# Kernel tuning notes

Measured on AMD Instinct MI355X. Metric: run time of the kernel, lower is better.

Reference implementation:

```python
import jax, jax.numpy as jnp
import numpy as np

N_EMBD = 1024
HEAD_SIZE = 128


def setup_inputs() -> dict:
    key = jax.random.key(0)
    k_x, k_w, k_cov, k_b = jax.random.split(key, 4)
    x = jax.random.normal(k_x, (16384, 2, N_EMBD), dtype=jnp.float32)
    # values_proj: nn.Linear(n_embd, head_size, bias=False) -> weight [head_size, n_embd]
    W = jax.random.normal(k_w, (HEAD_SIZE, N_EMBD), dtype=jnp.float32) * (N_EMBD ** -0.5)
    cov = jax.random.normal(k_cov, (HEAD_SIZE, HEAD_SIZE), dtype=jnp.float32) * (HEAD_SIZE ** -0.5)
    bias = jax.random.normal(k_b, (HEAD_SIZE,), dtype=jnp.float32)
    return {"x": x, "W": W, "cov": cov, "bias": bias}


def reference(x, W, cov, bias):
    # x: [B, 2, E]; W: [H, E]; cov: [H, H]; bias: [H]
    values = jnp.einsum('be,he->bh', x[:, 0, :], W)  # [B, H]
    mask = jnp.einsum('be,he->bh', x[:, 1, :], W)    # [B, H]
    # diag_embed(mask) @ cov == mask[:, :, None] * cov  -> [B, H, H]
    coeffs = jax.nn.softmax(mask[:, :, None] * cov[None, :, :], axis=-1)
    # values.unsqueeze(1) @ coeffs + bias, then [:, 0, :]
    out = jnp.einsum('bh,bhk->bk', values, coeffs) + bias
    return out
```

## Files before the change

kernel.cpp:

```cpp
#include <hip/hip_runtime.h>
#include <hip/hip_bf16.h>

#define LOG2E 1.4426950408889634f

typedef __attribute__((ext_vector_type(8))) short frag_ab;
typedef __attribute__((ext_vector_type(4))) float frag_cd;

__device__ inline short f2bf(float f) {
    union { float f; unsigned u; } v; v.f = f;
    unsigned r = v.u + 0x7fffu + ((v.u >> 16) & 1u);
    return (short)(r >> 16);
}

__global__ __launch_bounds__(256) void prep_kernel(const float* __restrict__ W,
                                                   const float* __restrict__ cov,
                                                   short* __restrict__ wbf,
                                                   float* __restrict__ rmm) {
    if (blockIdx.x < 64) {
        int g = blockIdx.x * 256 + threadIdx.x;
        int h = g >> 7;
        int k0 = (g & 127) << 3;
        const float* src = W + h * 1024 + k0;
        float4 w0 = *(const float4*)src;
        float4 w1 = *(const float4*)(src + 4);
        frag_ab af;
        af[0] = f2bf(w0.x); af[1] = f2bf(w0.y); af[2] = f2bf(w0.z); af[3] = f2bf(w0.w);
        af[4] = f2bf(w1.x); af[5] = f2bf(w1.y); af[6] = f2bf(w1.z); af[7] = f2bf(w1.w);
        int c = k0 >> 6, s = (k0 >> 5) & 1, kg = (k0 >> 3) & 3;
        int nt = h >> 4, m = h & 15, lane = kg * 16 + m;
        int dst = (((c * 8 + nt) * 2 + s) * 64 + lane) * 8;
        *(frag_ab*)(wbf + dst) = af;
    } else {
        int h = blockIdx.x - 64;
        int lane = threadIdx.x;
        if (lane < 64) {
            float c1 = cov[h * 128 + lane];
            float c2 = cov[h * 128 + 64 + lane];
            float mx = fmaxf(c1, c2), mn = fminf(c1, c2);
            for (int o = 1; o < 64; o <<= 1) {
                mx = fmaxf(mx, __shfl_xor(mx, o, 64));
                mn = fminf(mn, __shfl_xor(mn, o, 64));
            }
            if (lane == 0) { rmm[h] = LOG2E * mx; rmm[128 + h] = LOG2E * mn; }
        }
    }
}

__global__ __launch_bounds__(256, 2) void proj_kernel(const float* __restrict__ x,
                                                      const short* __restrict__ wbf,
                                                      float* __restrict__ vm) {
    __shared__ __align__(16) short Bs[2][8192];
    const int tid = threadIdx.x;
    const int lane = tid & 63, wave = tid >> 6;
    const int m = lane & 15, kg = lane >> 4;
    const long rowbase = (long)blockIdx.x * 64 + wave * 16;
    const float* xrow = x + (rowbase + m) * 1024 + kg * 8;

    frag_cd acc[8];
#pragma unroll
    for (int nt = 0; nt < 8; ++nt) acc[nt] = (frag_cd){0.f, 0.f, 0.f, 0.f};

    {
        const char* wc = (const char*)wbf;
        float4 t0 = *(const float4*)(wc + tid * 16);
        float4 t1 = *(const float4*)(wc + 4096 + tid * 16);
        float4 t2 = *(const float4*)(wc + 8192 + tid * 16);
        float4 t3 = *(const float4*)(wc + 12288 + tid * 16);
        char* bd = (char*)&Bs[0][0] + tid * 16;
        *(float4*)(bd)         = t0;
        *(float4*)(bd + 4096)  = t1;
        *(float4*)(bd + 8192)  = t2;
        *(float4*)(bd + 12288) = t3;
    }
    float4 a0 = *(const float4*)(xrow);
    float4 a1 = *(const float4*)(xrow + 4);
    float4 a2 = *(const float4*)(xrow + 32);
    float4 a3 = *(const float4*)(xrow + 36);
    __syncthreads();

    int cb = 0;
    for (int c = 0; c < 16; ++c) {
        float4 n0, n1, n2, n3, B0, B1, B2, B3;
        if (c < 15) {
            const float* xn = xrow + (c + 1) * 64;
            n0 = *(const float4*)(xn);
            n1 = *(const float4*)(xn + 4);
            n2 = *(const float4*)(xn + 32);
            n3 = *(const float4*)(xn + 36);
            const char* wc = (const char*)wbf + (c + 1) * 16384;
            B0 = *(const float4*)(wc + tid * 16);
            B1 = *(const float4*)(wc + 4096 + tid * 16);
            B2 = *(const float4*)(wc + 8192 + tid * 16);
            B3 = *(const float4*)(wc + 12288 + tid * 16);
        }
        frag_ab af0, af1;
        af0[0] = f2bf(a0.x); af0[1] = f2bf(a0.y); af0[2] = f2bf(a0.z); af0[3] = f2bf(a0.w);
        af0[4] = f2bf(a1.x); af0[5] = f2bf(a1.y); af0[6] = f2bf(a1.z); af0[7] = f2bf(a1.w);
        af1[0] = f2bf(a2.x); af1[1] = f2bf(a2.y); af1[2] = f2bf(a2.z); af1[3] = f2bf(a2.w);
        af1[4] = f2bf(a3.x); af1[5] = f2bf(a3.y); af1[6] = f2bf(a3.z); af1[7] = f2bf(a3.w);

        const char* bs = (const char*)&Bs[cb][0];
#pragma unroll
        for (int nt = 0; nt < 8; ++nt) {
            frag_ab bf0 = *(const frag_ab*)(bs + (nt * 2 + 0) * 1024 + lane * 16);
            acc[nt] = __builtin_amdgcn_mfma_f32_16x16x32_bf16(af0, bf0, acc[nt], 0, 0, 0);
            frag_ab bf1 = *(const frag_ab*)(bs + (nt * 2 + 1) * 1024 + lane * 16);
            acc[nt] = __builtin_amdgcn_mfma_f32_16x16x32_bf16(af1, bf1, acc[nt], 0, 0, 0);
        }
        if (c < 15) {
            char* bd = (char*)&Bs[cb ^ 1][0] + tid * 16;
            *(float4*)(bd)         = B0;
            *(float4*)(bd + 4096)  = B1;
            *(float4*)(bd + 8192)  = B2;
            *(float4*)(bd + 12288) = B3;
            a0 = n0; a1 = n1; a2 = n2; a3 = n3;
        }
        __syncthreads();
        cb ^= 1;
    }

#pragma unroll
    for (int nt = 0; nt < 8; ++nt) {
#pragma unroll
        for (int r = 0; r < 4; ++r) {
            long row = rowbase + kg * 4 + r;
            vm[row * 128 + nt * 16 + m] = acc[nt][r];
        }
    }
}

__global__ __launch_bounds__(512, 4) void combine_kernel(const float* __restrict__ vm,
                                                         const float* __restrict__ cov,
                                                         const float* __restrict__ bias,
                                                         const float* __restrict__ rmm,
                                                         float* __restrict__ out, int B) {
    __shared__ float mask_s[128], m2_s[128], v_s[128];
    __shared__ float obuf[32][132];
    const int t = threadIdx.x;
    const int i = t >> 4;
    const int j = t & 15;

    float covreg[4][8];
#pragma unroll
    for (int hh = 0; hh < 4; ++hh) {
        const float* cr = cov + (long)(i * 4 + hh) * 128 + j * 8;
        float4 c0 = *(const float4*)cr;
        float4 c1 = *(const float4*)(cr + 4);
        covreg[hh][0] = LOG2E * c0.x; covreg[hh][1] = LOG2E * c0.y;
        covreg[hh][2] = LOG2E * c0.z; covreg[hh][3] = LOG2E * c0.w;
        covreg[hh][4] = LOG2E * c1.x; covreg[hh][5] = LOG2E * c1.y;
        covreg[hh][6] = LOG2E * c1.z; covreg[hh][7] = LOG2E * c1.w;
    }
    float rmax_own = 0.f, rmin_own = 0.f, bias_own = 0.f;
    if (t < 128) {
        rmax_own = rmm[t];
        rmin_own = rmm[128 + t];
        bias_own = bias[t];
    }

    for (int b = blockIdx.x; b < B; b += gridDim.x) {
        if (t < 128) {
            float val = vm[(long)(2 * b) * 128 + t];
            float mk  = vm[(long)(2 * b + 1) * 128 + t];
            v_s[t] = val;
            mask_s[t] = mk;
            m2_s[t] = mk * (mk >= 0.f ? rmax_own : rmin_own);
        }
        __syncthreads();

        float op[8] = {0.f, 0.f, 0.f, 0.f, 0.f, 0.f, 0.f, 0.f};
#pragma unroll
        for (int hh = 0; hh < 4; ++hh) {
            float mh = mask_s[i * 4 + hh];
            float mm = m2_s[i * 4 + hh];
            float p[8];
            float lsum = 0.f;
#pragma unroll
            for (int kk = 0; kk < 8; ++kk) {
                float e = __builtin_amdgcn_exp2f(fmaf(mh, covreg[hh][kk], -mm));
                p[kk] = e;
                lsum += e;
            }
            lsum += __shfl_xor(lsum, 1, 16);
            lsum += __shfl_xor(lsum, 2, 16);
            lsum += __shfl_xor(lsum, 4, 16);
            lsum += __shfl_xor(lsum, 8, 16);
            float w = v_s[i * 4 + hh] * __builtin_amdgcn_rcpf(lsum);
#pragma unroll
            for (int kk = 0; kk < 8; ++kk) op[kk] = fmaf(w, p[kk], op[kk]);
        }
        *(float4*)&obuf[i][j * 8]     = make_float4(op[0], op[1], op[2], op[3]);
        *(float4*)&obuf[i][j * 8 + 4] = make_float4(op[4], op[5], op[6], op[7]);
        __syncthreads();

        if (t < 128) {
            float o = 0.f;
#pragma unroll
            for (int ii = 0; ii < 32; ++ii) o += obuf[ii][t];
            out[(long)b * 128 + t] = o + bias_own;
        }
        __syncthreads();
    }
}

extern "C" void kernel_launch(void* const* d_in, const int* in_sizes, int n_in,
                              void* d_out, int out_size, void* d_ws, size_t ws_size,
                              hipStream_t stream) {
    const float* x    = (const float*)d_in[0];
    const float* W    = (const float*)d_in[1];
    const float* cov  = (const float*)d_in[2];
    const float* bias = (const float*)d_in[3];
    float* out = (float*)d_out;

    const int B = in_sizes[0] / (2 * 1024);

    float* vm  = (float*)d_ws;
    short* wbf = (short*)(vm + (size_t)2 * B * 128);
    float* rmm = (float*)(wbf + 128 * 1024);

    prep_kernel<<<192, 256, 0, stream>>>(W, cov, wbf, rmm);

    const int blocks = (2 * B) / 64;
    proj_kernel<<<blocks, 256, 0, stream>>>(x, wbf, vm);

    combine_kernel<<<2048, 512, 0, stream>>>(vm, cov, bias, rmm, out, B);
}
```

Baseline: 273.1 us.

## Fuse projection GEMM and softmax-combine into one kernel via LDS staging

Merges the projection kernel and the combine kernel into a single kernel. Projected values and mask rows now go to LDS instead of a global workspace and are consumed in place, each block producing 32 batch outputs. This removes one kernel launch and the global write and re-read of the intermediate. The cross-lane softmax row sums now use DPP row-rotate adds instead of shuffles. In exchange, the combine phase is serialized behind the GEMM in each block, and register and LDS pressure grow (64 cov values per thread), which could reduce occupancy.

```diff
diff --git a/kernel.cpp b/kernel.cpp
--- a/kernel.cpp
+++ b/kernel.cpp
@@ -10,6 +10,12 @@
     union { float f; unsigned u; } v; v.f = f;
     unsigned r = v.u + 0x7fffu + ((v.u >> 16) & 1u);
     return (short)(r >> 16);
+}
+
+template<int CTRL>
+__device__ inline float dpp_ror_add(float x) {
+    int t = __builtin_amdgcn_update_dpp(0, __builtin_bit_cast(int, x), CTRL, 0xf, 0xf, false);
+    return x + __builtin_bit_cast(float, t);
 }
 
 __global__ __launch_bounds__(256) void prep_kernel(const float* __restrict__ W,
@@ -46,15 +52,23 @@
     }
 }
 
-__global__ __launch_bounds__(256, 2) void proj_kernel(const float* __restrict__ x,
-                                                      const short* __restrict__ wbf,
-                                                      float* __restrict__ vm) {
-    __shared__ __align__(16) short Bs[2][8192];
+__global__ __launch_bounds__(256, 2) void fused_kernel(const float* __restrict__ x,
+                                                       const short* __restrict__ wbf,
+                                                       const float* __restrict__ cov,
+                                                       const float* __restrict__ bias,
+                                                       const float* __restrict__ rmm,
+                                                       float* __restrict__ out) {
+    __shared__ __align__(16) char smem[64 * 132 * 4];
+    __shared__ float obuf[2][16][132];
+    __shared__ float bias_s[128];
+
     const int tid = threadIdx.x;
     const int lane = tid & 63, wave = tid >> 6;
     const int m = lane & 15, kg = lane >> 4;
     const long rowbase = (long)blockIdx.x * 64 + wave * 16;
     const float* xrow = x + (rowbase + m) * 1024 + kg * 8;
+
+    if (tid < 128) bias_s[tid] = bias[tid];
 
     frag_cd acc[8];
 #pragma unroll
@@ -66,7 +80,7 @@
         float4 t1 = *(const float4*)(wc + 4096 + tid * 16);
         float4 t2 = *(const float4*)(wc + 8192 + tid * 16);
         float4 t3 = *(const float4*)(wc + 12288 + tid * 16);
-        char* bd = (char*)&Bs[0][0] + tid * 16;
+        char* bd = smem + tid * 16;
         *(float4*)(bd)         = t0;
         *(float4*)(bd + 4096)  = t1;
         *(float4*)(bd + 8192)  = t2;
@@ -99,7 +113,7 @@
         af1[0] = f2bf(a2.x); af1[1] = f2bf(a2.y); af1[2] = f2bf(a2.z); af1[3] = f2bf(a2.w);
         af1[4] = f2bf(a3.x); af1[5] = f2bf(a3.y); af1[6] = f2bf(a3.z); af1[7] = f2bf(a3.w);
 
-        const char* bs = (const char*)&Bs[cb][0];
+        const char* bs = smem + cb * 16384;
 #pragma unroll
         for (int nt = 0; nt < 8; ++nt) {
             frag_ab bf0 = *(const frag_ab*)(bs + (nt * 2 + 0) * 1024 + lane * 16);
@@ -108,7 +122,7 @@
             acc[nt] = __builtin_amdgcn_mfma_f32_16x16x32_bf16(af1, bf1, acc[nt], 0, 0, 0);
         }
         if (c < 15) {
-            char* bd = (char*)&Bs[cb ^ 1][0] + tid * 16;
+            char* bd = smem + (cb ^ 1) * 16384 + tid * 16;
             *(float4*)(bd)         = B0;
             *(float4*)(bd + 4096)  = B1;
             *(float4*)(bd + 8192)  = B2;
@@ -119,31 +133,12 @@
         cb ^= 1;
     }
 
-#pragma unroll
-    for (int nt = 0; nt < 8; ++nt) {
-#pragma unroll
-        for (int r = 0; r < 4; ++r) {
-            long row = rowbase + kg * 4 + r;
-            vm[row * 128 + nt * 16 + m] = acc[nt][r];
-        }
-    }
-}
-
-__global__ __launch_bounds__(512, 4) void combine_kernel(const float* __restrict__ vm,
-                                                         const float* __restrict__ cov,
-                                                         const float* __restrict__ bias,
-                                                         const float* __restrict__ rmm,
-                                                         float* __restrict__ out, int B) {
-    __shared__ float mask_s[128], m2_s[128], v_s[128];
-    __shared__ float obuf[32][132];
-    const int t = threadIdx.x;
-    const int i = t >> 4;
-    const int j = t & 15;
-
-    float covreg[4][8];
-#pragma unroll
-    for (int hh = 0; hh < 4; ++hh) {
-        const float* cr = cov + (long)(i * 4 + hh) * 128 + j * 8;
+    const int i = tid >> 4;
+    const int j = tid & 15;
+    float covreg[8][8];
+#pragma unroll
+    for (int hh = 0; hh < 8; ++hh) {
+        const float* cr = cov + (long)(i * 8 + hh) * 128 + j * 8;
         float4 c0 = *(const float4*)cr;
         float4 c1 = *(const float4*)(cr + 4);
         covreg[hh][0] = LOG2E * c0.x; covreg[hh][1] = LOG2E * c0.y;
@@ -151,53 +146,66 @@
         covreg[hh][4] = LOG2E * c1.x; covreg[hh][5] = LOG2E * c1.y;
         covreg[hh][6] = LOG2E * c1.z; covreg[hh][7] = LOG2E * c1.w;
     }
-    float rmax_own = 0.f, rmin_own = 0.f, bias_own = 0.f;
-    if (t < 128) {
-        rmax_own = rmm[t];
-        rmin_own = rmm[128 + t];
-        bias_own = bias[t];
-    }
-
-    for (int b = blockIdx.x; b < B; b += gridDim.x) {
-        if (t < 128) {
-            float val = vm[(long)(2 * b) * 128 + t];
-            float mk  = vm[(long)(2 * b + 1) * 128 + t];
-            v_s[t] = val;
-            mask_s[t] = mk;
-            m2_s[t] = mk * (mk >= 0.f ? rmax_own : rmin_own);
+    float rmx[8], rmn[8];
+#pragma unroll
+    for (int hh = 0; hh < 8; ++hh) {
+        rmx[hh] = rmm[i * 8 + hh];
+        rmn[hh] = rmm[128 + i * 8 + hh];
+    }
+
+    float* vmf = (float*)smem;
+#pragma unroll
+    for (int nt = 0; nt < 8; ++nt)
+#pragma unroll
+        for (int r = 0; r < 4; ++r)
+            vmf[(wave * 16 + kg * 4 + r) * 132 + nt * 16 + m] = acc[nt][r];
+    __syncthreads();
+
+    const long outbase = (long)blockIdx.x * 32 * 128;
+    for (int bl2 = 0; bl2 < 16; ++bl2) {
+#pragma unroll
+        for (int sb = 0; sb < 2; ++sb) {
+            const int bl = bl2 * 2 + sb;
+            const float* vrow = vmf + (2 * bl) * 132 + i * 8;
+            const float* mrow = vmf + (2 * bl + 1) * 132 + i * 8;
+            float4 v0  = *(const float4*)(vrow);
+            float4 v1  = *(const float4*)(vrow + 4);
+            float4 mk0 = *(const float4*)(mrow);
+            float4 mk1 = *(const float4*)(mrow + 4);
+            float vh[8] = {v0.x, v0.y, v0.z, v0.w, v1.x, v1.y, v1.z, v1.w};
+            float mh[8] = {mk0.x, mk0.y, mk0.z, mk0.w, mk1.x, mk1.y, mk1.z, mk1.w};
+            float op[8] = {0.f, 0.f, 0.f, 0.f, 0.f, 0.f, 0.f, 0.f};
+#pragma unroll
+            for (int hh = 0; hh < 8; ++hh) {
+                float mv = mh[hh];
+                float mmax = mv * (mv >= 0.f ? rmx[hh] : rmn[hh]);
+                float p[8];
+                float lsum = 0.f;
+#pragma unroll
+                for (int kk = 0; kk < 8; ++kk) {
+                    float e = __builtin_amdgcn_exp2f(fmaf(mv, covreg[hh][kk], -mmax));
+                    p[kk] = e;
+                    lsum += e;
+                }
+                lsum = dpp_ror_add<0x121>(lsum);
+                lsum = dpp_ror_add<0x122>(lsum);
+                lsum = dpp_ror_add<0x124>(lsum);
+                lsum = dpp_ror_add<0x128>(lsum);
+                float w = vh[hh] * __builtin_amdgcn_rcpf(lsum);
+#pragma unroll
+                for (int kk = 0; kk < 8; ++kk) op[kk] = fmaf(w, p[kk], op[kk]);
+            }
+            *(float4*)&obuf[sb][i][j * 8]     = make_float4(op[0], op[1], op[2], op[3]);
+            *(float4*)&obuf[sb][i][j * 8 + 4] = make_float4(op[4], op[5], op[6], op[7]);
         }
         __syncthreads();
-
-        float op[8] = {0.f, 0.f, 0.f, 0.f, 0.f, 0.f, 0.f, 0.f};
-#pragma unroll
-        for (int hh = 0; hh < 4; ++hh) {
-            float mh = mask_s[i * 4 + hh];
-            float mm = m2_s[i * 4 + hh];
-            float p[8];
-            float lsum = 0.f;
-#pragma unroll
-            for (int kk = 0; kk < 8; ++kk) {
-                float e = __builtin_amdgcn_exp2f(fmaf(mh, covreg[hh][kk], -mm));
-                p[kk] = e;
-                lsum += e;
-            }
-            lsum += __shfl_xor(lsum, 1, 16);
-            lsum += __shfl_xor(lsum, 2, 16);
-            lsum += __shfl_xor(lsum, 4, 16);
-            lsum += __shfl_xor(lsum, 8, 16);
-            float w = v_s[i * 4 + hh] * __builtin_amdgcn_rcpf(lsum);
-#pragma unroll
-            for (int kk = 0; kk < 8; ++kk) op[kk] = fmaf(w, p[kk], op[kk]);
-        }
-        *(float4*)&obuf[i][j * 8]     = make_float4(op[0], op[1], op[2], op[3]);
-        *(float4*)&obuf[i][j * 8 + 4] = make_float4(op[4], op[5], op[6], op[7]);
-        __syncthreads();
-
-        if (t < 128) {
-            float o = 0.f;
-#pragma unroll
-            for (int ii = 0; ii < 32; ++ii) o += obuf[ii][t];
-            out[(long)b * 128 + t] = o + bias_own;
+        {
+            const int sb = tid >> 7;
+            const int k  = tid & 127;
+            float o = bias_s[k];
+#pragma unroll
+            for (int ii = 0; ii < 16; ++ii) o += obuf[sb][ii][k];
+            out[outbase + (bl2 * 2 + sb) * 128 + k] = o;
         }
         __syncthreads();
     }
@@ -214,14 +222,9 @@
 
     const int B = in_sizes[0] / (2 * 1024);
 
-    float* vm  = (float*)d_ws;
-    short* wbf = (short*)(vm + (size_t)2 * B * 128);
+    short* wbf = (short*)d_ws;
     float* rmm = (float*)(wbf + 128 * 1024);
 
     prep_kernel<<<192, 256, 0, stream>>>(W, cov, wbf, rmm);
-
-    const int blocks = (2 * B) / 64;
-    proj_kernel<<<blocks, 256, 0, stream>>>(x, wbf, vm);
-
-    combine_kernel<<<2048, 512, 0, stream>>>(vm, cov, bias, rmm, out, B);
-}
+    fused_kernel<<<(2 * B) / 64, 256, 0, stream>>>(x, wbf, cov, bias, rmm, out);
+}
```

New measurement: 256.2 us. 1.07x faster.
